# Kernel tuning notes

Hardware: AMD Instinct MI355X
Metric: run time of the kernel (lower is better)

The kernel has to match this reference:

```python
import jax, jax.numpy as jnp
import numpy as np

RAY_SAMPLE = 64

def make_posenc(d_hid, n_samples):
    pos = np.arange(n_samples, dtype=np.float64)[:, None]
    j = np.arange(d_hid)[None, :]
    angle = pos / np.power(10000.0, 2.0 * (j // 2) / d_hid)
    table = np.where(j % 2 == 0, np.sin(angle), np.cos(angle))
    return jnp.asarray(table, dtype=jnp.float32)[None]  # [1, n_samples, d_hid]

def setup_inputs() -> dict:
    key = jax.random.key(0)
    ks = jax.random.split(key, 8)
    V, S, D = 1024, RAY_SAMPLE, 256
    w_scale = 1.0 / np.sqrt(D)
    return {
        "q": jax.random.normal(ks[0], (V, S, D), jnp.float32),
        "k": jax.random.normal(ks[1], (V, S, D), jnp.float32),
        "v": jax.random.normal(ks[2], (V, S, D), jnp.float32),
        "Wq": jax.random.normal(ks[3], (D, D), jnp.float32) * w_scale,
        "Wk": jax.random.normal(ks[4], (D, D), jnp.float32) * w_scale,
        "Wv": jax.random.normal(ks[5], (D, D), jnp.float32) * w_scale,
        "Wo": jax.random.normal(ks[6], (D, D), jnp.float32) * w_scale,
        "bo": jnp.zeros((D,), jnp.float32),
    }

def reference(q, k, v, Wq, Wk, Wv, Wo, bo):
    views = k.shape[0]
    D = q.shape[-1]
    S = RAY_SAMPLE
    pe = make_posenc(D, S)  # [1, S, D]
    residual = q.reshape(-1, S, D)
    # projections (torch Linear: x @ W.T), reshape to ray blocks, add pos-enc
    qp = (q @ Wq.T).reshape(-1, S, D) + pe
    kp = (k @ Wk.T).reshape(-1, S, D) + pe
    vp = (v @ Wv.T).reshape(-1, S, D) + pe
    scale = 1.0 / np.sqrt(D).astype(np.float32)
    attn = jax.nn.softmax(jnp.einsum('bqd,bkd->bqk', qp, kp) * scale, axis=-1)
    out = jnp.einsum('bqk,bkd->bqd', attn, vp)
    x = jax.nn.gelu(out @ Wo.T + bo, approximate=False) + residual
    return x.reshape(views, -1, D)
```

## Files before the change

### kernel.cpp

```cpp
#include <hip/hip_runtime.h>
#include <math.h>

#define NVIEWS 1024
#define SS 64
#define DD 256
#define KAUG 320

typedef __bf16 bf16x8 __attribute__((ext_vector_type(8)));
typedef float f32x4 __attribute__((ext_vector_type(4)));
typedef unsigned short us4 __attribute__((ext_vector_type(4)));
typedef unsigned short us8 __attribute__((ext_vector_type(8)));
typedef unsigned int u32x4 __attribute__((ext_vector_type(4)));

#define STR_W 264
#define STR_T 72
#define OFF_A 0
#define OFF_B 36864
#define OFF_P 70656
#define LDS_TOTAL 79872

#define WS_WQ 0
#define WS_WK 81920
#define WS_WV 163840
#define WS_WO 245760

__device__ __forceinline__ unsigned short f2bf(float f) {
    return (unsigned short)((__builtin_bit_cast(unsigned int, f) + 0x8000u) >> 16);
}
__device__ __forceinline__ float bf2f(unsigned short h) {
    unsigned int u = ((unsigned int)h) << 16;
    return __builtin_bit_cast(float, u);
}
__device__ __forceinline__ unsigned int packbf2(float lo, float hi) {
    unsigned int ul = __builtin_bit_cast(unsigned int, lo) + 0x8000u;
    unsigned int uh = __builtin_bit_cast(unsigned int, hi) + 0x8000u;
    return __builtin_amdgcn_perm(uh, ul, 0x07060302u);
}

__global__ void prep_kernel(const float* __restrict__ Wq, const float* __restrict__ Wk,
                            const float* __restrict__ Wv, const float* __restrict__ Wo,
                            unsigned short* __restrict__ ws) {
    int t = blockIdx.x * blockDim.x + threadIdx.x;
    int n = t >> 8, k = t & 255;
    ws[WS_WQ + n * KAUG + k] = f2bf(Wq[t]);
    ws[WS_WK + n * KAUG + k] = f2bf(Wk[t]);
    ws[WS_WV + n * KAUG + k] = f2bf(Wv[t]);
    ws[WS_WO + t]            = f2bf(Wo[t]);
    if (t < SS * DD) {
        int j = t >> 8, d = t & 255;
        float ang = (float)j * expf(-((float)(d >> 1)) * (9.210340371976184f / 128.0f));
        unsigned short pb = f2bf((d & 1) ? cosf(ang) : sinf(ang));
        ws[WS_WQ + d * KAUG + 256 + j] = pb;
        ws[WS_WK + d * KAUG + 256 + j] = pb;
        ws[WS_WV + d * KAUG + 256 + j] = pb;
    }
}

#define LOAD_A_FRAG(dst, Xp, row, kk)                                          \
    {                                                                          \
        const float4* _p = (const float4*)((Xp) + (row) * DD + (kk));          \
        float4 _a = _p[0], _b = _p[1];                                         \
        u32x4 _w;                                                              \
        _w[0] = packbf2(_a.x, _a.y); _w[1] = packbf2(_a.z, _a.w);              \
        _w[2] = packbf2(_b.x, _b.y); _w[3] = packbf2(_b.z, _b.w);              \
        dst = __builtin_bit_cast(us8, _w);                                     \
    }

#define MFMA(d, a, b) d = __builtin_amdgcn_mfma_f32_16x16x32_bf16(             \
        __builtin_bit_cast(bf16x8, a), __builtin_bit_cast(bf16x8, b), d, 0, 0, 0)

#define PROJECT(Xp, Wp)                                                        \
    _Pragma("unroll 2")                                                        \
    for (int k0 = 0; k0 < DD; k0 += 32) {                                      \
        us8 af0, af1, af2, af3, bq0, bq1, bq2, bq3;                            \
        LOAD_A_FRAG(af0, Xp, l, k0 + koff);                                    \
        LOAD_A_FRAG(af1, Xp, 16 + l, k0 + koff);                               \
        LOAD_A_FRAG(af2, Xp, 32 + l, k0 + koff);                               \
        LOAD_A_FRAG(af3, Xp, 48 + l, k0 + koff);                               \
        bq0 = *(const us8*)((Wp) + (n0 + l) * KAUG + k0 + koff);               \
        bq1 = *(const us8*)((Wp) + (n0 + 16 + l) * KAUG + k0 + koff);          \
        bq2 = *(const us8*)((Wp) + (n0 + 32 + l) * KAUG + k0 + koff);          \
        bq3 = *(const us8*)((Wp) + (n0 + 48 + l) * KAUG + k0 + koff);          \
        MFMA(acc[0][0], af0, bq0); MFMA(acc[0][1], af0, bq1);                  \
        MFMA(acc[0][2], af0, bq2); MFMA(acc[0][3], af0, bq3);                  \
        MFMA(acc[1][0], af1, bq0); MFMA(acc[1][1], af1, bq1);                  \
        MFMA(acc[1][2], af1, bq2); MFMA(acc[1][3], af1, bq3);                  \
        MFMA(acc[2][0], af2, bq0); MFMA(acc[2][1], af2, bq1);                  \
        MFMA(acc[2][2], af2, bq2); MFMA(acc[2][3], af2, bq3);                  \
        MFMA(acc[3][0], af3, bq0); MFMA(acc[3][1], af3, bq1);                  \
        MFMA(acc[3][2], af3, bq2); MFMA(acc[3][3], af3, bq3);                  \
    }                                                                          \
    {                                                                          \
         \
        us8 p0 = *(const us8*)((Wp) + (n0 + l) * KAUG + 256 + koff);           \
        us8 p1 = *(const us8*)((Wp) + (n0 + 16 + l) * KAUG + 256 + koff);      \
        us8 p2 = *(const us8*)((Wp) + (n0 + 32 + l) * KAUG + 256 + koff);      \
        us8 p3 = *(const us8*)((Wp) + (n0 + 48 + l) * KAUG + 256 + koff);      \
        us8 r0 = *(const us8*)((Wp) + (n0 + l) * KAUG + 288 + koff);           \
        us8 r1 = *(const us8*)((Wp) + (n0 + 16 + l) * KAUG + 288 + koff);      \
        us8 r2 = *(const us8*)((Wp) + (n0 + 32 + l) * KAUG + 288 + koff);      \
        us8 r3 = *(const us8*)((Wp) + (n0 + 48 + l) * KAUG + 288 + koff);      \
        MFMA(acc[0][0], idA, p0); MFMA(acc[0][1], idA, p1);                    \
        MFMA(acc[0][2], idA, p2); MFMA(acc[0][3], idA, p3);                    \
        MFMA(acc[1][0], idB, p0); MFMA(acc[1][1], idB, p1);                    \
        MFMA(acc[1][2], idB, p2); MFMA(acc[1][3], idB, p3);                    \
        MFMA(acc[2][0], idA, r0); MFMA(acc[2][1], idA, r1);                    \
        MFMA(acc[2][2], idA, r2); MFMA(acc[2][3], idA, r3);                    \
        MFMA(acc[3][0], idB, r0); MFMA(acc[3][1], idB, r1);                    \
        MFMA(acc[3][2], idB, r2); MFMA(acc[3][3], idB, r3);                    \
    }

#define ZERO_ACC                                                               \
    _Pragma("unroll")                                                          \
    for (int _i = 0; _i < 4; ++_i)                                             \
        _Pragma("unroll")                                                      \
        for (int _j = 0; _j < 4; ++_j) acc[_i][_j] = (f32x4){0.f, 0.f, 0.f, 0.f};

#define STORE_C(dst)                                                           \
    _Pragma("unroll")                                                          \
    for (int mt = 0; mt < 4; ++mt)                                             \
        _Pragma("unroll")                                                      \
        for (int nt = 0; nt < 4; ++nt) {                                       \
            int col = n0 + nt * 16 + l;                                        \
            _Pragma("unroll")                                                  \
            for (int r = 0; r < 4; ++r)                                        \
                (dst)[(mt * 16 + (quad << 2) + r) * STR_W + col] = f2bf(acc[mt][nt][r]); \
        }

__global__ __launch_bounds__(256, 2)
void attn_kernel(const float* __restrict__ qg_, const float* __restrict__ kg_,
                 const float* __restrict__ vg_, const unsigned short* __restrict__ ws,
                 const float* __restrict__ bo, float* __restrict__ outg) {
    __shared__ __attribute__((aligned(16))) char smem[LDS_TOTAL];
    unsigned short* sA = (unsigned short*)(smem + OFF_A);
    unsigned short* sB = (unsigned short*)(smem + OFF_B);
    unsigned short* sP = (unsigned short*)(smem + OFF_P);

    const unsigned short* Wq = ws + WS_WQ;
    const unsigned short* Wk = ws + WS_WK;
    const unsigned short* Wv = ws + WS_WV;
    const unsigned short* Wo = ws + WS_WO;

    const int tid  = threadIdx.x;
    const int w    = tid >> 6;
    const int lane = tid & 63;
    const int quad = lane >> 4;
    const int l    = lane & 15;
    const int n0   = w << 6;
    const int koff = quad << 3;

    unsigned int w1 = (l & 1) ? 0x3F800000u : 0x00003F80u;
    int dw = (l >> 1) & 3;
    bool cA = (quad == (l >> 3));
    bool cB = (quad == 2 + (l >> 3));
    u32x4 eA, eB;
    eA[0] = (cA && dw == 0) ? w1 : 0u; eA[1] = (cA && dw == 1) ? w1 : 0u;
    eA[2] = (cA && dw == 2) ? w1 : 0u; eA[3] = (cA && dw == 3) ? w1 : 0u;
    eB[0] = (cB && dw == 0) ? w1 : 0u; eB[1] = (cB && dw == 1) ? w1 : 0u;
    eB[2] = (cB && dw == 2) ? w1 : 0u; eB[3] = (cB && dw == 3) ? w1 : 0u;
    us8 idA = __builtin_bit_cast(us8, eA);
    us8 idB = __builtin_bit_cast(us8, eB);

    const size_t base = (size_t)blockIdx.x * (SS * DD);
    const float* qg = qg_ + base;
    const float* kg = kg_ + base;
    const float* vg = vg_ + base;
    float* og = outg + base;

    f32x4 acc[4][4];

    ZERO_ACC
    PROJECT(kg, Wk)
    STORE_C(sB)

    ZERO_ACC
    PROJECT(qg, Wq)
    STORE_C(sA)

    __syncthreads();

    {
        f32x4 s0 = {0.f,0.f,0.f,0.f}, s1 = {0.f,0.f,0.f,0.f};
        f32x4 s2 = {0.f,0.f,0.f,0.f}, s3 = {0.f,0.f,0.f,0.f};
        #pragma unroll
        for (int k0 = 0; k0 < DD; k0 += 32) {
            us8 a  = *(const us8*)(sA + (w * 16 + l) * STR_W + k0 + koff);
            us8 b0 = *(const us8*)(sB + (l) * STR_W + k0 + koff);
            us8 b1 = *(const us8*)(sB + (16 + l) * STR_W + k0 + koff);
            us8 b2 = *(const us8*)(sB + (32 + l) * STR_W + k0 + koff);
            us8 b3 = *(const us8*)(sB + (48 + l) * STR_W + k0 + koff);
            MFMA(s0, a, b0); MFMA(s1, a, b1); MFMA(s2, a, b2); MFMA(s3, a, b3);
        }
        #pragma unroll
        for (int r = 0; r < 4; ++r) {
            float v0 = s0[r] * 0.0625f, v1 = s1[r] * 0.0625f;
            float v2 = s2[r] * 0.0625f, v3 = s3[r] * 0.0625f;
            float mx = fmaxf(fmaxf(v0, v1), fmaxf(v2, v3));
            #pragma unroll
            for (int d = 1; d <= 8; d <<= 1) mx = fmaxf(mx, __shfl_xor(mx, d));
            float e0 = __expf(v0 - mx), e1 = __expf(v1 - mx);
            float e2 = __expf(v2 - mx), e3 = __expf(v3 - mx);
            float sm = e0 + e1 + e2 + e3;
            #pragma unroll
            for (int d = 1; d <= 8; d <<= 1) sm += __shfl_xor(sm, d);
            float inv = 1.0f / sm;
            int row = w * 16 + (quad << 2) + r;
            sP[row * STR_T + l]      = f2bf(e0 * inv);
            sP[row * STR_T + 16 + l] = f2bf(e1 * inv);
            sP[row * STR_T + 32 + l] = f2bf(e2 * inv);
            sP[row * STR_T + 48 + l] = f2bf(e3 * inv);
        }
    }

    ZERO_ACC
    PROJECT(vg, Wv)
    __syncthreads();
    #pragma unroll
    for (int mt = 0; mt < 4; ++mt)
        #pragma unroll
        for (int nt = 0; nt < 4; ++nt) {
            int col = n0 + nt * 16 + l;
            int rbase = mt * 16 + (quad << 2);
            us4 pk;
            #pragma unroll
            for (int r = 0; r < 4; ++r)
                pk[r] = f2bf(acc[mt][nt][r]);
            *(us4*)(sA + col * STR_T + rbase) = pk;
        }
    __syncthreads();

    {
        ZERO_ACC
        #pragma unroll
        for (int k0 = 0; k0 < 64; k0 += 32) {
            us8 a0 = *(const us8*)(sP + (l) * STR_T + k0 + koff);
            us8 a1 = *(const us8*)(sP + (16 + l) * STR_T + k0 + koff);
            us8 a2 = *(const us8*)(sP + (32 + l) * STR_T + k0 + koff);
            us8 a3 = *(const us8*)(sP + (48 + l) * STR_T + k0 + koff);
            us8 b0 = *(const us8*)(sA + (n0 + l) * STR_T + k0 + koff);
            us8 b1 = *(const us8*)(sA + (n0 + 16 + l) * STR_T + k0 + koff);
            us8 b2 = *(const us8*)(sA + (n0 + 32 + l) * STR_T + k0 + koff);
            us8 b3 = *(const us8*)(sA + (n0 + 48 + l) * STR_T + k0 + koff);
            MFMA(acc[0][0], a0, b0); MFMA(acc[0][1], a0, b1);
            MFMA(acc[0][2], a0, b2); MFMA(acc[0][3], a0, b3);
            MFMA(acc[1][0], a1, b0); MFMA(acc[1][1], a1, b1);
            MFMA(acc[1][2], a1, b2); MFMA(acc[1][3], a1, b3);
            MFMA(acc[2][0], a2, b0); MFMA(acc[2][1], a2, b1);
            MFMA(acc[2][2], a2, b2); MFMA(acc[2][3], a2, b3);
            MFMA(acc[3][0], a3, b0); MFMA(acc[3][1], a3, b1);
            MFMA(acc[3][2], a3, b2); MFMA(acc[3][3], a3, b3);
        }
        #pragma unroll
        for (int mt = 0; mt < 4; ++mt)
            #pragma unroll
            for (int nt = 0; nt < 4; ++nt) {
                int col = n0 + nt * 16 + l;
                #pragma unroll
                for (int r = 0; r < 4; ++r)
                    sB[(mt * 16 + (quad << 2) + r) * STR_W + col] = f2bf(acc[mt][nt][r]);
            }
    }
    __syncthreads();

    {
        ZERO_ACC
        #pragma unroll 2
        for (int k0 = 0; k0 < DD; k0 += 32) {
            us8 a0 = *(const us8*)(sB + (l) * STR_W + k0 + koff);
            us8 a1 = *(const us8*)(sB + (16 + l) * STR_W + k0 + koff);
            us8 a2 = *(const us8*)(sB + (32 + l) * STR_W + k0 + koff);
            us8 a3 = *(const us8*)(sB + (48 + l) * STR_W + k0 + koff);
            us8 b0 = *(const us8*)(Wo + (n0 + l) * DD + k0 + koff);
            us8 b1 = *(const us8*)(Wo + (n0 + 16 + l) * DD + k0 + koff);
            us8 b2 = *(const us8*)(Wo + (n0 + 32 + l) * DD + k0 + koff);
            us8 b3 = *(const us8*)(Wo + (n0 + 48 + l) * DD + k0 + koff);
            MFMA(acc[0][0], a0, b0); MFMA(acc[0][1], a0, b1);
            MFMA(acc[0][2], a0, b2); MFMA(acc[0][3], a0, b3);
            MFMA(acc[1][0], a1, b0); MFMA(acc[1][1], a1, b1);
            MFMA(acc[1][2], a1, b2); MFMA(acc[1][3], a1, b3);
            MFMA(acc[2][0], a2, b0); MFMA(acc[2][1], a2, b1);
            MFMA(acc[2][2], a2, b2); MFMA(acc[2][3], a2, b3);
            MFMA(acc[3][0], a3, b0); MFMA(acc[3][1], a3, b1);
            MFMA(acc[3][2], a3, b2); MFMA(acc[3][3], a3, b3);
        }
        #pragma unroll
        for (int nt = 0; nt < 4; ++nt) {
            int col = n0 + nt * 16 + l;
            float bias = bo[col];
            #pragma unroll
            for (int mt = 0; mt < 4; ++mt) {
                #pragma unroll
                for (int r = 0; r < 4; ++r) {
                    int row = mt * 16 + (quad << 2) + r;
                    float y = acc[mt][nt][r] + bias;
                    float u = 1.5957691216f * y * (1.0f + 0.044715f * y * y);
                    float g = y / (1.0f + __expf(-u));
                    sA[row * STR_W + col] = f2bf(g);
                }
            }
        }
    }
    __syncthreads();

    #pragma unroll
    for (int s = 0; s < 16; ++s) {
        int f = s * 1024 + tid * 4;
        int row = f >> 8, col = f & 255;
        us4 gb = *(const us4*)(sA + row * STR_W + col);
        float4 qv = *(const float4*)(qg + f);
        float4 o;
        o.x = bf2f(gb[0]) + qv.x;
        o.y = bf2f(gb[1]) + qv.y;
        o.z = bf2f(gb[2]) + qv.z;
        o.w = bf2f(gb[3]) + qv.w;
        *(float4*)(og + f) = o;
    }
}

extern "C" void kernel_launch(void* const* d_in, const int* in_sizes, int n_in,
                              void* d_out, int out_size, void* d_ws, size_t ws_size,
                              hipStream_t stream) {
    const float* q  = (const float*)d_in[0];
    const float* k  = (const float*)d_in[1];
    const float* v  = (const float*)d_in[2];
    const float* Wq = (const float*)d_in[3];
    const float* Wk = (const float*)d_in[4];
    const float* Wv = (const float*)d_in[5];
    const float* Wo = (const float*)d_in[6];
    const float* bo = (const float*)d_in[7];
    unsigned short* ws = (unsigned short*)d_ws;

    prep_kernel<<<256, 256, 0, stream>>>(Wq, Wk, Wv, Wo, ws);
    attn_kernel<<<NVIEWS, 256, 0, stream>>>(q, k, v, ws, bo, (float*)d_out);
}
```

Baseline: 334.1 us.

## Double block to 512 threads, split projections and GEMMs across wave halves

The attention kernel now launches 512 threads (8 waves) per view instead of 256. The K and Q projections run concurrently on the two wave halves. V projection overlaps with QK^T/softmax on the lower half, and the PV and output GEMMs split the N dimension into 32-column slices per wave. This aims to raise per-block parallelism and latency hiding. In exchange it adds register pressure under the launch_bounds(512,4) constraint, and LDS usage may limit occupancy.

```diff
diff --git a/kernel.cpp b/kernel.cpp
--- a/kernel.cpp
+++ b/kernel.cpp
@@ -127,7 +127,7 @@
                 (dst)[(mt * 16 + (quad << 2) + r) * STR_W + col] = f2bf(acc[mt][nt][r]); \
         }
 
-__global__ __launch_bounds__(256, 2)
+__global__ __launch_bounds__(512, 4)
 void attn_kernel(const float* __restrict__ qg_, const float* __restrict__ kg_,
                  const float* __restrict__ vg_, const unsigned short* __restrict__ ws,
                  const float* __restrict__ bo, float* __restrict__ outg) {
@@ -143,10 +143,13 @@
 
     const int tid  = threadIdx.x;
     const int w    = tid >> 6;
+    const int wp   = w & 3;
+    const int whi  = w >> 2;
     const int lane = tid & 63;
     const int quad = lane >> 4;
     const int l    = lane & 15;
-    const int n0   = w << 6;
+    const int n0   = wp << 6;
+    const int n0h  = w << 5;
     const int koff = quad << 3;
 
     unsigned int w1 = (l & 1) ? 0x3F800000u : 0x00003F80u;
@@ -169,17 +172,17 @@
 
     f32x4 acc[4][4];
 
-    ZERO_ACC
-    PROJECT(kg, Wk)
-    STORE_C(sB)
-
-    ZERO_ACC
-    PROJECT(qg, Wq)
-    STORE_C(sA)
-
-    __syncthreads();
-
     {
+        const float* X1          = whi ? qg : kg;
+        const unsigned short* W1 = whi ? Wq : Wk;
+        unsigned short* D1       = whi ? sA : sB;
+        ZERO_ACC
+        PROJECT(X1, W1)
+        STORE_C(D1)
+    }
+    __syncthreads();
+
+    if (whi == 0) {
         f32x4 s0 = {0.f,0.f,0.f,0.f}, s1 = {0.f,0.f,0.f,0.f};
         f32x4 s2 = {0.f,0.f,0.f,0.f}, s3 = {0.f,0.f,0.f,0.f};
         #pragma unroll
@@ -210,23 +213,26 @@
             sP[row * STR_T + 32 + l] = f2bf(e2 * inv);
             sP[row * STR_T + 48 + l] = f2bf(e3 * inv);
         }
-    }
-
-    ZERO_ACC
-    PROJECT(vg, Wv)
-    __syncthreads();
-    #pragma unroll
-    for (int mt = 0; mt < 4; ++mt)
-        #pragma unroll
-        for (int nt = 0; nt < 4; ++nt) {
-            int col = n0 + nt * 16 + l;
-            int rbase = mt * 16 + (quad << 2);
-            us4 pk;
-            #pragma unroll
-            for (int r = 0; r < 4; ++r)
-                pk[r] = f2bf(acc[mt][nt][r]);
-            *(us4*)(sA + col * STR_T + rbase) = pk;
-        }
+    } else {
+        ZERO_ACC
+        PROJECT(vg, Wv)
+    }
+    __syncthreads();
+
+    if (whi) {
+        #pragma unroll
+        for (int mt = 0; mt < 4; ++mt)
+            #pragma unroll
+            for (int nt = 0; nt < 4; ++nt) {
+                int col = n0 + nt * 16 + l;
+                int rbase = mt * 16 + (quad << 2);
+                us4 pk;
+                #pragma unroll
+                for (int r = 0; r < 4; ++r)
+                    pk[r] = f2bf(acc[mt][nt][r]);
+                *(us4*)(sA + col * STR_T + rbase) = pk;
+            }
+    }
     __syncthreads();
 
     {
@@ -237,24 +243,18 @@
             us8 a1 = *(const us8*)(sP + (16 + l) * STR_T + k0 + koff);
             us8 a2 = *(const us8*)(sP + (32 + l) * STR_T + k0 + koff);
             us8 a3 = *(const us8*)(sP + (48 + l) * STR_T + k0 + koff);
-            us8 b0 = *(const us8*)(sA + (n0 + l) * STR_T + k0 + koff);
-            us8 b1 = *(const us8*)(sA + (n0 + 16 + l) * STR_T + k0 + koff);
-            us8 b2 = *(const us8*)(sA + (n0 + 32 + l) * STR_T + k0 + koff);
-            us8 b3 = *(const us8*)(sA + (n0 + 48 + l) * STR_T + k0 + koff);
+            us8 b0 = *(const us8*)(sA + (n0h + l) * STR_T + k0 + koff);
+            us8 b1 = *(const us8*)(sA + (n0h + 16 + l) * STR_T + k0 + koff);
             MFMA(acc[0][0], a0, b0); MFMA(acc[0][1], a0, b1);
-            MFMA(acc[0][2], a0, b2); MFMA(acc[0][3], a0, b3);
             MFMA(acc[1][0], a1, b0); MFMA(acc[1][1], a1, b1);
-            MFMA(acc[1][2], a1, b2); MFMA(acc[1][3], a1, b3);
             MFMA(acc[2][0], a2, b0); MFMA(acc[2][1], a2, b1);
-            MFMA(acc[2][2], a2, b2); MFMA(acc[2][3], a2, b3);
             MFMA(acc[3][0], a3, b0); MFMA(acc[3][1], a3, b1);
-            MFMA(acc[3][2], a3, b2); MFMA(acc[3][3], a3, b3);
         }
         #pragma unroll
         for (int mt = 0; mt < 4; ++mt)
             #pragma unroll
-            for (int nt = 0; nt < 4; ++nt) {
-                int col = n0 + nt * 16 + l;
+            for (int nt = 0; nt < 2; ++nt) {
+                int col = n0h + nt * 16 + l;
                 #pragma unroll
                 for (int r = 0; r < 4; ++r)
                     sB[(mt * 16 + (quad << 2) + r) * STR_W + col] = f2bf(acc[mt][nt][r]);
@@ -270,22 +270,16 @@
             us8 a1 = *(const us8*)(sB + (16 + l) * STR_W + k0 + koff);
             us8 a2 = *(const us8*)(sB + (32 + l) * STR_W + k0 + koff);
             us8 a3 = *(const us8*)(sB + (48 + l) * STR_W + k0 + koff);
-            us8 b0 = *(const us8*)(Wo + (n0 + l) * DD + k0 + koff);
-            us8 b1 = *(const us8*)(Wo + (n0 + 16 + l) * DD + k0 + koff);
-            us8 b2 = *(const us8*)(Wo + (n0 + 32 + l) * DD + k0 + koff);
-            us8 b3 = *(const us8*)(Wo + (n0 + 48 + l) * DD + k0 + koff);
+            us8 b0 = *(const us8*)(Wo + (n0h + l) * DD + k0 + koff);
+            us8 b1 = *(const us8*)(Wo + (n0h + 16 + l) * DD + k0 + koff);
             MFMA(acc[0][0], a0, b0); MFMA(acc[0][1], a0, b1);
-            MFMA(acc[0][2], a0, b2); MFMA(acc[0][3], a0, b3);
             MFMA(acc[1][0], a1, b0); MFMA(acc[1][1], a1, b1);
-            MFMA(acc[1][2], a1, b2); MFMA(acc[1][3], a1, b3);
             MFMA(acc[2][0], a2, b0); MFMA(acc[2][1], a2, b1);
-            MFMA(acc[2][2], a2, b2); MFMA(acc[2][3], a2, b3);
             MFMA(acc[3][0], a3, b0); MFMA(acc[3][1], a3, b1);
-            MFMA(acc[3][2], a3, b2); MFMA(acc[3][3], a3, b3);
-        }
-        #pragma unroll
-        for (int nt = 0; nt < 4; ++nt) {
-            int col = n0 + nt * 16 + l;
+        }
+        #pragma unroll
+        for (int nt = 0; nt < 2; ++nt) {
+            int col = n0h + nt * 16 + l;
             float bias = bo[col];
             #pragma unroll
             for (int mt = 0; mt < 4; ++mt) {
@@ -303,8 +297,8 @@
     __syncthreads();
 
     #pragma unroll
-    for (int s = 0; s < 16; ++s) {
-        int f = s * 1024 + tid * 4;
+    for (int s = 0; s < 8; ++s) {
+        int f = s * 2048 + tid * 4;
         int row = f >> 8, col = f & 255;
         us4 gb = *(const us4*)(sA + row * STR_W + col);
         float4 qv = *(const float4*)(qg + f);
@@ -328,8 +322,9 @@
     const float* Wv = (const float*)d_in[5];
     const float* Wo = (const float*)d_in[6];
     const float* bo = (const float*)d_in[7];
+    const float* bo_ = bo; (void)bo_;
     unsigned short* ws = (unsigned short*)d_ws;
 
     prep_kernel<<<256, 256, 0, stream>>>(Wq, Wk, Wv, Wo, ws);
-    attn_kernel<<<NVIEWS, 256, 0, stream>>>(q, k, v, ws, bo, (float*)d_out);
-}
+    attn_kernel<<<NVIEWS, 512, 0, stream>>>(q, k, v, ws, bo, (float*)d_out);
+}
```

After: 347.8 us. 1.04x slower.
